# Kernel tuning notes

Hardware: AMD Instinct MI355X
Metric: run time of the kernel (lower is better)

The kernel has to match this reference:

```python
import jax, jax.numpy as jnp
import numpy as np

B, S, D, H = 2, 2048, 2048, 16
HD = D // H
FF = 4 * D
EPS = 1e-5
SCALE = 1.0 / np.sqrt(D)  # source uses 1/sqrt(d_out), not 1/sqrt(head_dim)


def _gelu_tanh(x):
    c = np.sqrt(2.0 / np.pi).astype(np.float32)
    return 0.5 * x * (1.0 + jnp.tanh(c * (x + 0.044715 * x * x * x)))


def _layernorm(x, scale, shift):
    mean = jnp.mean(x, axis=-1, keepdims=True)
    var = jnp.mean(jnp.square(x - mean), axis=-1, keepdims=True)  # correction=0
    return (x - mean) * jax.lax.rsqrt(var + EPS) * scale + shift


def setup_inputs() -> dict:
    key = jax.random.key(0)
    ks = jax.random.split(key, 10)
    init = lambda k, shape, fan_in: (jax.random.normal(k, shape, jnp.float32) / np.sqrt(fan_in))
    return {
        "x": jax.random.normal(ks[0], (B, S, D), jnp.float32),
        "wq": init(ks[1], (D, D), D),
        "wk": init(ks[2], (D, D), D),
        "wv": init(ks[3], (D, D), D),
        "wo": init(ks[4], (D, D), D),
        "bo": jnp.zeros((D,), jnp.float32),
        "g1": jnp.ones((D,), jnp.float32),
        "s1": jnp.zeros((D,), jnp.float32),
        "g2": jnp.ones((D,), jnp.float32),
        "s2": jnp.zeros((D,), jnp.float32),
        "w1": init(ks[5], (D, FF), D),
        "b1": jnp.zeros((FF,), jnp.float32),
        "w2": init(ks[6], (FF, D), FF),
        "b2": jnp.zeros((D,), jnp.float32),
    }


def _block(x, wq, wk, wv, wo, bo, g1, s1, g2, s2, w1, b1, w2, b2):
    # pre-LN attention
    h = _layernorm(x, g1, s1)
    q = (h @ wq).reshape(B, S, H, HD).transpose(0, 2, 1, 3)  # [B,H,S,HD]
    k = (h @ wk).reshape(B, S, H, HD).transpose(0, 2, 1, 3)
    v = (h @ wv).reshape(B, S, H, HD).transpose(0, 2, 1, 3)
    scores = jnp.einsum('bhqd,bhkd->bhqk', q, k) * SCALE
    causal = jnp.tril(jnp.ones((S, S), dtype=bool))  # mask strictly-upper
    scores = jnp.where(causal, scores, -jnp.inf)
    attn = jax.nn.softmax(scores, axis=-1)
    ctx = jnp.einsum('bhqk,bhkd->bhqd', attn, v)
    ctx = ctx.transpose(0, 2, 1, 3).reshape(B, S, D)
    x = x + ctx @ wo + bo
    # pre-LN FFN
    h = _layernorm(x, g2, s2)
    h = _gelu_tanh(h @ w1 + b1) @ w2 + b2
    return x + h


def reference(x, wq, wk, wv, wo, bo, g1, s1, g2, s2, w1, b1, w2, b2):
    return _block(x, wq, wk, wv, wo, bo, g1, s1, g2, s2, w1, b1, w2, b2)
```

## Files before the change

### kernel.cpp

```cpp
#include <hip/hip_runtime.h>
#include <hip/hip_bf16.h>
#include <cstdint>

constexpr float SCALE_QK = 0.02209708691207961f;
constexpr float LOG2E    = 1.4426950408889634f;

using short8 = __attribute__((ext_vector_type(8))) short;
using f32x4  = __attribute__((ext_vector_type(4))) float;
using ushort4v = __attribute__((ext_vector_type(4))) ushort;

#define MFMA16(a,b,c) __builtin_amdgcn_mfma_f32_16x16x32_bf16((a),(b),(c),0,0,0)

__device__ __forceinline__ ushort f2bf(float f){
  uint32_t u = __builtin_bit_cast(uint32_t, f);
  u += 0x7fffu + ((u >> 16) & 1u);
  return (ushort)(u >> 16);
}

__device__ __forceinline__ void gload_lds16(const void* g, void* l){
  __builtin_amdgcn_global_load_lds(
      (const __attribute__((address_space(1))) void*)g,
      (__attribute__((address_space(3))) void*)l, 16, 0, 0);
}

__global__ __launch_bounds__(256) void ln_kernel(
    const float* __restrict__ x, const float* __restrict__ g,
    const float* __restrict__ sh, ushort* __restrict__ out){
  const int row = blockIdx.x, t = threadIdx.x;
  const float* xr = x + (size_t)row*2048 + t*8;
  float v[8];
  *(float4*)&v[0] = *(const float4*)(xr);
  *(float4*)&v[4] = *(const float4*)(xr + 4);
  float s = 0.f, sq = 0.f;
#pragma unroll
  for (int i = 0; i < 8; ++i){ s += v[i]; sq += v[i]*v[i]; }
#pragma unroll
  for (int d = 1; d < 64; d <<= 1){ s += __shfl_xor(s, d, 64); sq += __shfl_xor(sq, d, 64); }
  __shared__ float red[8];
  const int w = t >> 6, lane = t & 63;
  if (lane == 0){ red[w] = s; red[4 + w] = sq; }
  __syncthreads();
  s  = red[0] + red[1] + red[2] + red[3];
  sq = red[4] + red[5] + red[6] + red[7];
  const float mean = s * (1.f/2048.f);
  const float inv  = rsqrtf(sq * (1.f/2048.f) - mean*mean + 1e-5f);
  union { ushort u[8]; uint4 v4; } o;
#pragma unroll
  for (int i = 0; i < 8; ++i){
    int j = t*8 + i;
    o.u[i] = f2bf((v[i] - mean) * inv * g[j] + sh[j]);
  }
  *(uint4*)(out + (size_t)row*2048 + t*8) = o.v4;
}

__global__ __launch_bounds__(256) void wconv4(
    const float* __restrict__ w0, const float* __restrict__ w1p,
    const float* __restrict__ w2p, const float* __restrict__ w3p,
    ushort* __restrict__ out){
  __shared__ ushort tile[32][34];
  const int tx = threadIdx.x & 31, ty = threadIdx.x >> 5;
  const int n0 = blockIdx.x * 32, k0 = blockIdx.y * 32, z = blockIdx.z;
  const float* in = (z == 0) ? w0 : (z == 1) ? w1p : (z == 2) ? w2p : w3p;
  ushort* o = out + (size_t)z * 4194304;
#pragma unroll
  for (int r = 0; r < 4; ++r){
    int kk = ty + r*8;
    tile[kk][tx] = f2bf(in[(size_t)(k0 + kk)*2048 + n0 + tx]);
  }
  __syncthreads();
#pragma unroll
  for (int r = 0; r < 4; ++r){
    int nn = ty + r*8;
    o[(size_t)(n0 + nn)*2048 + k0 + tx] = tile[tx][nn];
  }
}

__global__ __launch_bounds__(256) void wconv_ffn(
    const float* __restrict__ w1, const float* __restrict__ w2,
    ushort* __restrict__ w1T, ushort* __restrict__ w2T){
  __shared__ ushort tile[32][34];
  const int tx = threadIdx.x & 31, ty = threadIdx.x >> 5;
  const int z = blockIdx.z;
  const float* in; ushort* out; int K, N, n0, k0;
  if (z == 0){ in = w1; out = w1T; K = 2048; N = 8192;
               n0 = blockIdx.x * 32; k0 = blockIdx.y * 32; }
  else       { in = w2; out = w2T; K = 8192; N = 2048;
               n0 = blockIdx.y * 32; k0 = blockIdx.x * 32; }
#pragma unroll
  for (int r = 0; r < 4; ++r){
    int kk = ty + r*8;
    tile[kk][tx] = f2bf(in[(size_t)(k0 + kk)*N + n0 + tx]);
  }
  __syncthreads();
#pragma unroll
  for (int r = 0; r < 4; ++r){
    int nn = ty + r*8;
    out[(size_t)(n0 + nn)*K + k0 + tx] = tile[tx][nn];
  }
}

template<int EPI>
__global__ __launch_bounds__(256) void gemm_bt(
    const ushort* __restrict__ A, const ushort* __restrict__ Bt,
    int N, int K, void* __restrict__ outp,
    const float* __restrict__ resid, const float* __restrict__ bias){
  __shared__ ushort lds[2][128*64];
  const int tid = threadIdx.x, lane = tid & 63, wid = tid >> 6;
  const int wr = wid >> 1, wc = wid & 1;
  const int l15 = lane & 15, l4 = lane >> 4;

  const int bid = blockIdx.x;
  const int xcd = bid & 7, j = bid >> 3;
  const int mb = xcd*4 + (j & 3);
  const int nb = j >> 2;
  const int m0 = mb * 128, n0 = nb * 128;

  f32x4 acc[4][4];
#pragma unroll
  for (int mi = 0; mi < 4; ++mi)
#pragma unroll
    for (int ni = 0; ni < 4; ++ni) acc[mi][ni] = (f32x4){0.f,0.f,0.f,0.f};

  const ushort* Abase = A  + (size_t)m0*K;
  const ushort* Bbase = Bt + (size_t)n0*K;

  const int NTk = K >> 6;
  for (int kt = 0; kt < NTk; ++kt){
    if (kt) __syncthreads();
#pragma unroll
    for (int i = 0; i < 4; ++i){
      const int chunk = (i*4 + wid)*64 + lane;
      const int row = chunk >> 3;
      const int c8  = (chunk & 7) ^ (row & 7);
      const size_t goff = (size_t)row*K + (size_t)kt*64 + c8*8;
      gload_lds16(Abase + goff, (ushort*)&lds[0][0] + (size_t)(i*4 + wid)*512);
      gload_lds16(Bbase + goff, (ushort*)&lds[1][0] + (size_t)(i*4 + wid)*512);
    }
    __syncthreads();

#pragma unroll
    for (int kk = 0; kk < 2; ++kk){
      short8 af[4], bf[4];
      const int kb = kk*4 + l4;
#pragma unroll
      for (int i = 0; i < 4; ++i){
        const int rA = wr*64 + i*16 + l15;
        af[i] = *(const short8*)&lds[0][rA*64 + ((kb ^ (rA & 7))*8)];
        const int rB = wc*64 + i*16 + l15;
        bf[i] = *(const short8*)&lds[1][rB*64 + ((kb ^ (rB & 7))*8)];
      }
#pragma unroll
      for (int mi = 0; mi < 4; ++mi)
#pragma unroll
        for (int ni = 0; ni < 4; ++ni)
          acc[mi][ni] = MFMA16(af[mi], bf[ni], acc[mi][ni]);
    }
  }

  if constexpr (EPI == 0){
    __syncthreads();
    ushort* tile = (ushort*)&lds[0][0];
    const int which = n0 >> 11;
    const int hh = (n0 & 2047) >> 7;
    const int bb = m0 >> 11, srow0 = m0 & 2047;
    if (which != 2){
      const float qs = (which == 0) ? SCALE_QK * LOG2E : 1.0f;
#pragma unroll
      for (int mi = 0; mi < 4; ++mi)
#pragma unroll
        for (int ni = 0; ni < 4; ++ni){
          const int rl = wr*64 + mi*16 + l4*4;
          const int cl = wc*64 + ni*16 + l15;
#pragma unroll
          for (int j2 = 0; j2 < 4; ++j2)
            tile[(rl + j2)*128 + cl] = f2bf(acc[mi][ni][j2] * qs);
        }
      __syncthreads();
      ushort* dst = (ushort*)outp + (size_t)which*8388608 +
                    ((size_t)(bb*16 + hh)*2048 + srow0)*128;
#pragma unroll
      for (int i = 0; i < 8; ++i){
        const int c = i*256 + tid, row = c >> 4, d8 = (c & 15)*8;
        *(uint4*)(dst + (size_t)row*128 + d8) = *(const uint4*)&tile[row*128 + d8];
      }
    } else {
#pragma unroll
      for (int mi = 0; mi < 4; ++mi)
#pragma unroll
        for (int ni = 0; ni < 4; ++ni){
          const int rl = wr*64 + mi*16 + l4*4;
          const int cl = wc*64 + ni*16 + l15;
          ushort4v o;
#pragma unroll
          for (int j2 = 0; j2 < 4; ++j2) o[j2] = f2bf(acc[mi][ni][j2]);
          *(ushort4v*)&tile[cl*128 + rl] = o;
        }
      __syncthreads();
      ushort* dst = (ushort*)outp + (size_t)2*8388608 +
                    (size_t)(bb*16 + hh)*262144 + srow0;
#pragma unroll
      for (int i = 0; i < 8; ++i){
        const int c = i*256 + tid, drow = c >> 4, s8 = (c & 15)*8;
        *(uint4*)(dst + (size_t)drow*2048 + s8) = *(const uint4*)&tile[drow*128 + s8];
      }
    }
  } else {
#pragma unroll
    for (int mi = 0; mi < 4; ++mi){
#pragma unroll
      for (int ni = 0; ni < 4; ++ni){
        const int rloc = wr*64 + mi*16 + l4*4;
        const int col  = n0 + wc*64 + ni*16 + l15;
#pragma unroll
        for (int j2 = 0; j2 < 4; ++j2){
          const int m = m0 + rloc + j2;
          float v = acc[mi][ni][j2];
          if constexpr (EPI == 1){
            ((float*)outp)[(size_t)m*N + col] = resid[(size_t)m*N + col] + bias[col] + v;
          } else {
            const float xx = v + bias[col];
            const float z  = 0.7978845608f*(xx + 0.044715f*xx*xx*xx);
            const float t  = __expf(-2.f*fabsf(z));
            const float th = (1.f - t)/(1.f + t);
            const float gl = 0.5f*xx*(1.f + copysignf(th, xx));
            ((ushort*)outp)[(size_t)m*N + col] = f2bf(gl);
          }
        }
      }
    }
  }
}

__global__ __launch_bounds__(512, 2) void attn_kernel(
    const ushort* __restrict__ q, const ushort* __restrict__ k,
    const ushort* __restrict__ vt, ushort* __restrict__ ctx){
  __shared__ ushort k_lds[2][64*128];
  __shared__ ushort v_lds[2][128*64];
  __shared__ ushort p_lds[8][16*64];
  const int tid = threadIdx.x, lane = tid & 63, w = tid >> 6;
  const int l15 = lane & 15, l4 = lane >> 4;
  const int id = blockIdx.x;
  const int bh = id & 31;
  const int r  = id >> 5;
  const int qt = (r < 8) ? (15 - r) : (r - 8);
  const int bb = bh >> 4, hh = bh & 15;
  const ushort* kbase = k  + (size_t)bh * 262144;
  const ushort* vbase = vt + (size_t)bh * 262144;

  short8 qf[4];
  {
    const int s = qt*128 + w*16 + l15;
    const ushort* qr = q + ((size_t)bh*2048 + s)*128 + l4*8;
#pragma unroll
    for (int kk = 0; kk < 4; ++kk) qf[kk] = *(const short8*)(qr + kk*32);
  }

  f32x4 cacc[8];
#pragma unroll
  for (int dt = 0; dt < 8; ++dt) cacc[dt] = (f32x4){0.f,0.f,0.f,0.f};
  float mrun[4], lrun[4];
#pragma unroll
  for (int j = 0; j < 4; ++j){ mrun[j] = -1e30f; lrun[j] = 0.f; }

  auto stage = [&](int buf, int t){
    const ushort* ksrc = kbase + (size_t)t*8192;
#pragma unroll
    for (int i = 0; i < 2; ++i){
      const int base = i*512 + w*64;
      const int chunk = base + lane;
      const int kr = chunk >> 4;
      const int c8 = (chunk & 15) ^ (kr & 7);
      gload_lds16(ksrc + (size_t)kr*128 + c8*8, &k_lds[buf][(size_t)base*8]);
    }
#pragma unroll
    for (int i = 0; i < 2; ++i){
      const int base = i*512 + w*64;
      const int chunk = base + lane;
      const int vr = chunk >> 3;
      const int c8 = (chunk & 7) ^ (vr & 7);
      gload_lds16(vbase + (size_t)vr*2048 + t*64 + c8*8, &v_lds[buf][(size_t)base*8]);
    }
  };

  const int nt = 2*qt + 2;
  stage(0, 0);
  __syncthreads();
  int cur = 0;
  for (int t = 0; t < nt; ++t){
    if (t + 1 < nt) stage(cur ^ 1, t + 1);

    const bool skip = (t == 2*qt + 1) && (w < 4);
    if (!skip){
      f32x4 sa[4];
#pragma unroll
      for (int ct = 0; ct < 4; ++ct) sa[ct] = (f32x4){0.f,0.f,0.f,0.f};
      __builtin_amdgcn_s_setprio(1);
#pragma unroll
      for (int kk = 0; kk < 4; ++kk){
#pragma unroll
        for (int ct = 0; ct < 4; ++ct){
          const int kr = ct*16 + l15;
          short8 kf = *(const short8*)&k_lds[cur][kr*128 + (((kk*4 + l4) ^ (kr & 7))*8)];
          sa[ct] = MFMA16(qf[kk], kf, sa[ct]);
        }
      }
      __builtin_amdgcn_s_setprio(0);

      const bool anymask = (t >= 2*qt) && !((t == 2*qt) && (w >= 4));
      float rowlm[4];
      bool over = false;
#pragma unroll
      for (int j = 0; j < 4; ++j){
        const int qa = qt*128 + w*16 + l4*4 + j;
        float lm = -1e30f;
#pragma unroll
        for (int ct = 0; ct < 4; ++ct){
          float sc = sa[ct][j];
          if (anymask){
            const int ka = t*64 + ct*16 + l15;
            sc = (ka > qa) ? -1e30f : sc;
          }
          sa[ct][j] = sc;
          lm = fmaxf(lm, sc);
        }
        rowlm[j] = lm;
        over = over || (lm > mrun[j] + 8.f);
      }
      if (__any(over)){
#pragma unroll
        for (int j = 0; j < 4; ++j){
          float mx = rowlm[j];
#pragma unroll
          for (int d = 1; d < 16; d <<= 1) mx = fmaxf(mx, __shfl_xor(mx, d, 16));
          const float mnew = fmaxf(mrun[j], mx);
          const float corr = exp2f(mrun[j] - mnew);
          mrun[j] = mnew; lrun[j] *= corr;
#pragma unroll
          for (int dt = 0; dt < 8; ++dt) cacc[dt][j] *= corr;
        }
      }
#pragma unroll
      for (int j = 0; j < 4; ++j){
        float psum = 0.f;
#pragma unroll
        for (int ct = 0; ct < 4; ++ct){
          const float p = exp2f(sa[ct][j] - mrun[j]);
          sa[ct][j] = p; psum += p;
        }
        lrun[j] += psum;
      }

#pragma unroll
      for (int ct = 0; ct < 4; ++ct)
#pragma unroll
        for (int j = 0; j < 4; ++j){
          const int row = l4*4 + j, col = ct*16 + l15;
          p_lds[w][row*64 + ((col >> 3) ^ (row & 7))*8 + (col & 7)] = f2bf(sa[ct][j]);
        }

      __builtin_amdgcn_s_setprio(1);
#pragma unroll
      for (int kk2 = 0; kk2 < 2; ++kk2){
        const int kb = kk2*4 + l4;
        short8 pa = *(const short8*)&p_lds[w][l15*64 + ((kb ^ (l15 & 7))*8)];
#pragma unroll
        for (int dt = 0; dt < 8; ++dt){
          const int vr = dt*16 + l15;
          short8 vf = *(const short8*)&v_lds[cur][vr*64 + ((kb ^ (vr & 7))*8)];
          cacc[dt] = MFMA16(pa, vf, cacc[dt]);
        }
      }
      __builtin_amdgcn_s_setprio(0);
    }

    if (t + 1 < nt){ __syncthreads(); cur ^= 1; }
  }

  float inv[4];
#pragma unroll
  for (int j = 0; j < 4; ++j){
    float lt = lrun[j];
#pragma unroll
    for (int d = 1; d < 16; d <<= 1) lt += __shfl_xor(lt, d, 16);
    inv[j] = 1.f / lt;
  }
#pragma unroll
  for (int dt = 0; dt < 8; ++dt)
#pragma unroll
    for (int j = 0; j < 4; ++j){
      const int s = qt*128 + w*16 + l4*4 + j;
      const int d = dt*16 + l15;
      ctx[((size_t)(bb*2048 + s))*2048 + hh*128 + d] = f2bf(cacc[dt][j] * inv[j]);
    }
}

extern "C" void kernel_launch(void* const* d_in, const int* in_sizes, int n_in,
                              void* d_out, int out_size, void* d_ws, size_t ws_size,
                              hipStream_t stream) {
  const float* x  = (const float*)d_in[0];
  const float* wq = (const float*)d_in[1];
  const float* wk = (const float*)d_in[2];
  const float* wv = (const float*)d_in[3];
  const float* wo = (const float*)d_in[4];
  const float* bo = (const float*)d_in[5];
  const float* g1 = (const float*)d_in[6];
  const float* s1 = (const float*)d_in[7];
  const float* g2 = (const float*)d_in[8];
  const float* s2 = (const float*)d_in[9];
  const float* w1 = (const float*)d_in[10];
  const float* b1 = (const float*)d_in[11];
  const float* w2 = (const float*)d_in[12];
  const float* b2 = (const float*)d_in[13];
  float* out = (float*)d_out;
  char* ws = (char*)d_ws;

  ushort* wqkvT = (ushort*)(ws + 0);
  ushort* woT = (ushort*)(ws + 25165824);
  ushort* w1T = (ushort*)(ws + 33554432);
  ushort* w2T = (ushort*)(ws + 67108864);
  ushort* h1  = (ushort*)(ws + 100663296);
  ushort* qb  = (ushort*)(ws + 117440512);
  ushort* kb  = (ushort*)(ws + 134217728);
  ushort* vtb = (ushort*)(ws + 150994944);
  ushort* ctxb= (ushort*)(ws + 184549376);
  float*  x2  = (float*)(ws + 201326592);
  ushort* h2  = (ushort*)(ws + 234881024);
  ushort* ffb = (ushort*)(ws + 117440512);

  wconv4<<<dim3(64, 64, 4), 256, 0, stream>>>(wq, wk, wv, wo, wqkvT);
  wconv_ffn<<<dim3(256, 64, 2), 256, 0, stream>>>(w1, w2, w1T, w2T);

  ln_kernel<<<4096, 256, 0, stream>>>(x, g1, s1, h1);

  gemm_bt<0><<<32*48, 256, 0, stream>>>(h1, wqkvT, 6144, 2048, qb, nullptr, nullptr);

  attn_kernel<<<512, 512, 0, stream>>>(qb, kb, vtb, ctxb);

  gemm_bt<1><<<32*16, 256, 0, stream>>>(ctxb, woT, 2048, 2048, x2, x, bo);

  ln_kernel<<<4096, 256, 0, stream>>>(x2, g2, s2, h2);

  gemm_bt<2><<<32*64, 256, 0, stream>>>(h2, w1T, 8192, 2048, ffb, nullptr, b1);
  gemm_bt<1><<<32*16, 256, 0, stream>>>(ffb, w2T, 2048, 8192, out, x2, b2);

  (void)in_sizes; (void)n_in; (void)out_size; (void)ws_size;
}
```

Measured before the change: 676.3 us.

## Use 128-key tiles in attention and remap block order for FFN down GEMM

The attention kernel now stages 128-key K/V tiles per iteration instead of 64. This halves the number of loop iterations, barriers and online-softmax rescale passes, and drops the per-wave skip logic. LDS use rises to about 160 KB, so launch bounds drop to one block per CU, which lowers occupancy. Separately, the final K=8192 GEMM gets a new block-to-tile mapping that groups tiles per XCD differently, aiming at better L2 reuse.

```diff
diff --git a/kernel.cpp b/kernel.cpp
--- a/kernel.cpp
+++ b/kernel.cpp
@@ -99,7 +99,7 @@
   }
 }
 
-template<int EPI>
+template<int EPI, int MODE>
 __global__ __launch_bounds__(256) void gemm_bt(
     const ushort* __restrict__ A, const ushort* __restrict__ Bt,
     int N, int K, void* __restrict__ outp,
@@ -111,8 +111,14 @@
 
   const int bid = blockIdx.x;
   const int xcd = bid & 7, j = bid >> 3;
-  const int mb = xcd*4 + (j & 3);
-  const int nb = j >> 2;
+  int mb, nb;
+  if constexpr (MODE == 0){
+    mb = xcd*4 + (j & 3); nb = j >> 2;
+  } else {
+    const int jm = j & 1, rest = j >> 1;
+    nb = rest & 15;
+    mb = (rest >> 4)*16 + xcd*2 + jm;
+  }
   const int m0 = mb * 128, n0 = nb * 128;
 
   f32x4 acc[4][4];
@@ -231,11 +237,11 @@
   }
 }
 
-__global__ __launch_bounds__(512, 2) void attn_kernel(
+__global__ __launch_bounds__(512, 1) void attn_kernel(
     const ushort* __restrict__ q, const ushort* __restrict__ k,
     const ushort* __restrict__ vt, ushort* __restrict__ ctx){
-  __shared__ ushort k_lds[2][64*128];
-  __shared__ ushort v_lds[2][128*64];
+  __shared__ ushort k_lds[2][128*128];
+  __shared__ ushort v_lds[2][128*128];
   __shared__ ushort p_lds[8][16*64];
   const int tid = threadIdx.x, lane = tid & 63, w = tid >> 6;
   const int l15 = lane & 15, l4 = lane >> 4;
@@ -263,102 +269,101 @@
   for (int j = 0; j < 4; ++j){ mrun[j] = -1e30f; lrun[j] = 0.f; }
 
   auto stage = [&](int buf, int t){
-    const ushort* ksrc = kbase + (size_t)t*8192;
-#pragma unroll
-    for (int i = 0; i < 2; ++i){
-      const int base = i*512 + w*64;
-      const int chunk = base + lane;
+    const ushort* ksrc = kbase + (size_t)t*16384;
+#pragma unroll
+    for (int i = 0; i < 4; ++i){
+      const int chunk = i*512 + tid;
       const int kr = chunk >> 4;
       const int c8 = (chunk & 15) ^ (kr & 7);
-      gload_lds16(ksrc + (size_t)kr*128 + c8*8, &k_lds[buf][(size_t)base*8]);
-    }
-#pragma unroll
-    for (int i = 0; i < 2; ++i){
-      const int base = i*512 + w*64;
-      const int chunk = base + lane;
-      const int vr = chunk >> 3;
-      const int c8 = (chunk & 7) ^ (vr & 7);
-      gload_lds16(vbase + (size_t)vr*2048 + t*64 + c8*8, &v_lds[buf][(size_t)base*8]);
+      gload_lds16(ksrc + (size_t)kr*128 + c8*8, &k_lds[buf][(size_t)chunk*8]);
+    }
+#pragma unroll
+    for (int i = 0; i < 4; ++i){
+      const int chunk = i*512 + tid;
+      const int vr = chunk >> 4;
+      const int c8 = (chunk & 15) ^ (vr & 7);
+      gload_lds16(vbase + (size_t)vr*2048 + t*128 + c8*8, &v_lds[buf][(size_t)chunk*8]);
     }
   };
 
-  const int nt = 2*qt + 2;
+  const int nt = qt + 1;
   stage(0, 0);
   __syncthreads();
   int cur = 0;
   for (int t = 0; t < nt; ++t){
     if (t + 1 < nt) stage(cur ^ 1, t + 1);
 
-    const bool skip = (t == 2*qt + 1) && (w < 4);
-    if (!skip){
-      f32x4 sa[4];
-#pragma unroll
-      for (int ct = 0; ct < 4; ++ct) sa[ct] = (f32x4){0.f,0.f,0.f,0.f};
-      __builtin_amdgcn_s_setprio(1);
-#pragma unroll
-      for (int kk = 0; kk < 4; ++kk){
-#pragma unroll
-        for (int ct = 0; ct < 4; ++ct){
-          const int kr = ct*16 + l15;
-          short8 kf = *(const short8*)&k_lds[cur][kr*128 + (((kk*4 + l4) ^ (kr & 7))*8)];
-          sa[ct] = MFMA16(qf[kk], kf, sa[ct]);
-        }
-      }
-      __builtin_amdgcn_s_setprio(0);
-
-      const bool anymask = (t >= 2*qt) && !((t == 2*qt) && (w >= 4));
-      float rowlm[4];
-      bool over = false;
+    f32x4 sa[8];
+#pragma unroll
+    for (int ct = 0; ct < 8; ++ct) sa[ct] = (f32x4){0.f,0.f,0.f,0.f};
+    __builtin_amdgcn_s_setprio(1);
+#pragma unroll
+    for (int kk = 0; kk < 4; ++kk){
+#pragma unroll
+      for (int ct = 0; ct < 8; ++ct){
+        const int kr = ct*16 + l15;
+        short8 kf = *(const short8*)&k_lds[cur][kr*128 + (((kk*4 + l4) ^ (kr & 7))*8)];
+        sa[ct] = MFMA16(qf[kk], kf, sa[ct]);
+      }
+    }
+    __builtin_amdgcn_s_setprio(0);
+
+    const bool anymask = (t == qt);
+    float rowlm[4];
+    bool over = false;
+#pragma unroll
+    for (int j = 0; j < 4; ++j){
+      const int qa = qt*128 + w*16 + l4*4 + j;
+      float lm = -1e30f;
+#pragma unroll
+      for (int ct = 0; ct < 8; ++ct){
+        float sc = sa[ct][j];
+        if (anymask){
+          const int ka = t*128 + ct*16 + l15;
+          sc = (ka > qa) ? -1e30f : sc;
+        }
+        sa[ct][j] = sc;
+        lm = fmaxf(lm, sc);
+      }
+      rowlm[j] = lm;
+      over = over || (lm > mrun[j] + 8.f);
+    }
+    if (__any(over)){
 #pragma unroll
       for (int j = 0; j < 4; ++j){
-        const int qa = qt*128 + w*16 + l4*4 + j;
-        float lm = -1e30f;
-#pragma unroll
-        for (int ct = 0; ct < 4; ++ct){
-          float sc = sa[ct][j];
-          if (anymask){
-            const int ka = t*64 + ct*16 + l15;
-            sc = (ka > qa) ? -1e30f : sc;
-          }
-          sa[ct][j] = sc;
-          lm = fmaxf(lm, sc);
-        }
-        rowlm[j] = lm;
-        over = over || (lm > mrun[j] + 8.f);
-      }
-      if (__any(over)){
+        float mx = rowlm[j];
+#pragma unroll
+        for (int d = 1; d < 16; d <<= 1) mx = fmaxf(mx, __shfl_xor(mx, d, 16));
+        const float mnew = fmaxf(mrun[j], mx);
+        const float corr = exp2f(mrun[j] - mnew);
+        mrun[j] = mnew; lrun[j] *= corr;
+#pragma unroll
+        for (int dt = 0; dt < 8; ++dt) cacc[dt][j] *= corr;
+      }
+    }
+#pragma unroll
+    for (int j = 0; j < 4; ++j){
+      float psum = 0.f;
+#pragma unroll
+      for (int ct = 0; ct < 8; ++ct){
+        const float p = exp2f(sa[ct][j] - mrun[j]);
+        sa[ct][j] = p; psum += p;
+      }
+      lrun[j] += psum;
+    }
+
+    __builtin_amdgcn_s_setprio(1);
+#pragma unroll
+    for (int half = 0; half < 2; ++half){
+#pragma unroll
+      for (int ct2 = 0; ct2 < 4; ++ct2){
+        const int ct = half*4 + ct2;
 #pragma unroll
         for (int j = 0; j < 4; ++j){
-          float mx = rowlm[j];
-#pragma unroll
-          for (int d = 1; d < 16; d <<= 1) mx = fmaxf(mx, __shfl_xor(mx, d, 16));
-          const float mnew = fmaxf(mrun[j], mx);
-          const float corr = exp2f(mrun[j] - mnew);
-          mrun[j] = mnew; lrun[j] *= corr;
-#pragma unroll
-          for (int dt = 0; dt < 8; ++dt) cacc[dt][j] *= corr;
-        }
-      }
-#pragma unroll
-      for (int j = 0; j < 4; ++j){
-        float psum = 0.f;
-#pragma unroll
-        for (int ct = 0; ct < 4; ++ct){
-          const float p = exp2f(sa[ct][j] - mrun[j]);
-          sa[ct][j] = p; psum += p;
-        }
-        lrun[j] += psum;
-      }
-
-#pragma unroll
-      for (int ct = 0; ct < 4; ++ct)
-#pragma unroll
-        for (int j = 0; j < 4; ++j){
-          const int row = l4*4 + j, col = ct*16 + l15;
+          const int row = l4*4 + j, col = ct2*16 + l15;
           p_lds[w][row*64 + ((col >> 3) ^ (row & 7))*8 + (col & 7)] = f2bf(sa[ct][j]);
         }
-
-      __builtin_amdgcn_s_setprio(1);
+      }
 #pragma unroll
       for (int kk2 = 0; kk2 < 2; ++kk2){
         const int kb = kk2*4 + l4;
@@ -366,12 +371,13 @@
 #pragma unroll
         for (int dt = 0; dt < 8; ++dt){
           const int vr = dt*16 + l15;
-          short8 vf = *(const short8*)&v_lds[cur][vr*64 + ((kb ^ (vr & 7))*8)];
+          const int g = half*8 + kb;
+          short8 vf = *(const short8*)&v_lds[cur][vr*128 + ((g ^ (vr & 7))*8)];
           cacc[dt] = MFMA16(pa, vf, cacc[dt]);
         }
       }
-      __builtin_amdgcn_s_setprio(0);
-    }
+    }
+    __builtin_amdgcn_s_setprio(0);
 
     if (t + 1 < nt){ __syncthreads(); cur ^= 1; }
   }
@@ -432,16 +438,16 @@
 
   ln_kernel<<<4096, 256, 0, stream>>>(x, g1, s1, h1);
 
-  gemm_bt<0><<<32*48, 256, 0, stream>>>(h1, wqkvT, 6144, 2048, qb, nullptr, nullptr);
+  gemm_bt<0,0><<<32*48, 256, 0, stream>>>(h1, wqkvT, 6144, 2048, qb, nullptr, nullptr);
 
   attn_kernel<<<512, 512, 0, stream>>>(qb, kb, vtb, ctxb);
 
-  gemm_bt<1><<<32*16, 256, 0, stream>>>(ctxb, woT, 2048, 2048, x2, x, bo);
+  gemm_bt<1,0><<<32*16, 256, 0, stream>>>(ctxb, woT, 2048, 2048, x2, x, bo);
 
   ln_kernel<<<4096, 256, 0, stream>>>(x2, g2, s2, h2);
 
-  gemm_bt<2><<<32*64, 256, 0, stream>>>(h2, w1T, 8192, 2048, ffb, nullptr, b1);
-  gemm_bt<1><<<32*16, 256, 0, stream>>>(ffb, w2T, 2048, 8192, out, x2, b2);
+  gemm_bt<2,0><<<32*64, 256, 0, stream>>>(h2, w1T, 8192, 2048, ffb, nullptr, b1);
+  gemm_bt<1,1><<<32*16, 256, 0, stream>>>(ffb, w2T, 2048, 8192, out, x2, b2);
 
   (void)in_sizes; (void)n_in; (void)out_size; (void)ws_size;
 }
```

New measurement: 668.3 us. No clear change (-1.2%).
